# Optimization experiments

Hardware: AMD Instinct MI355X
Metric: run time of the kernel (lower is better)

The kernel has to match this reference:

```python
import jax, jax.numpy as jnp
import numpy as np

B, T, D, H = 128, 1024, 128, 128

def setup_inputs() -> dict:
    key = jax.random.key(0)
    ks = jax.random.split(key, 7)
    scale = 0.05
    return {
        "x": jax.random.normal(ks[0], (B, T, D), dtype=jnp.float32),
        "h0": jnp.zeros((B, H), dtype=jnp.float32),
        "U": jax.random.normal(ks[1], (D, H), dtype=jnp.float32) * scale,
        "W": jax.random.normal(ks[2], (H, H), dtype=jnp.float32) * scale,
        "V": jax.random.normal(ks[3], (H, H), dtype=jnp.float32) * scale,
        "bu": jnp.zeros((H,), dtype=jnp.float32),
        "bw": jnp.zeros((H,), dtype=jnp.float32),
        "bv": jnp.zeros((H,), dtype=jnp.float32),
    }

def reference(x, h0, U, W, V, bu, bw, bv):
    # Precompute input projection for all timesteps in one big GEMM: [B,T,H]
    xu = jnp.einsum('btd,dh->bth', x, U) + bu

    def step(h, xu_t):
        # st = tanh(x@U + bu + h@W + bw)
        st = jnp.tanh(xu_t + h @ W + bw)
        # o = tanh(st@V + bv)
        o = jnp.tanh(st @ V + bv)
        return st, o

    # scan over time: xu transposed to [T,B,H]
    _, o_seq = jax.lax.scan(step, h0, jnp.swapaxes(xu, 0, 1))
    return jnp.swapaxes(o_seq, 0, 1)  # [B,T,H]
```

## Files before the change

kernel.cpp:

```cpp
#include <hip/hip_runtime.h>

#define B_ 128
#define T_ 1024
#define D_ 128
#define H_ 128

typedef short bf16x8 __attribute__((ext_vector_type(8)));
typedef float f32x4 __attribute__((ext_vector_type(4)));

__device__ inline short f2bf(float f) {
    union { float f; unsigned u; } v; v.f = f;
    unsigned u = v.u;
    unsigned r = (u + 0x7fffu + ((u >> 16) & 1u)) >> 16;
    return (short)r;
}

__device__ inline float fast_tanh(float x) {
    float e = __expf(2.0f * x);
    return 1.0f - __fdividef(2.0f, 1.0f + e);
}

__device__ inline void lds_barrier() {
    asm volatile("s_waitcnt lgkmcnt(0)\n\ts_barrier" ::: "memory");
}

__global__ __launch_bounds__(256) void xu_kernel(
    const float* __restrict__ x, const float* __restrict__ U,
    const float* __restrict__ bu, float* __restrict__ out)
{
    __shared__ bf16x8 uf[2048];
    const int tid  = threadIdx.x;
    const int lane = tid & 63;
    const int wave = tid >> 6;
    const int q = lane >> 4, c = lane & 15;

    for (int s = tid; s < 2048; s += 256) {
        int l = s & 63, kk = (s >> 6) & 3, nt = s >> 8;
        int lq = l >> 4, lc = l & 15;
        int kbase = 32 * kk + 8 * lq;
        int col = 16 * nt + lc;
        bf16x8 f;
#pragma unroll
        for (int j = 0; j < 8; ++j)
            f[j] = f2bf(U[(kbase + j) * H_ + col]);
        uf[s] = f;
    }

    float bub[8];
#pragma unroll
    for (int nt = 0; nt < 8; ++nt) bub[nt] = bu[16 * nt + c];

    __syncthreads();

    for (int it = 0; it < 4; ++it) {
        const int row0 = (blockIdx.x * 4 + it) * 64 + wave * 16;

        bf16x8 af[4];
#pragma unroll
        for (int kk = 0; kk < 4; ++kk) {
            const float* px = x + (row0 + (lane & 15)) * D_ + 32 * kk + 8 * q;
            f32x4 a0 = *(const f32x4*)px;
            f32x4 a1 = *(const f32x4*)(px + 4);
            bf16x8 f;
            f[0] = f2bf(a0[0]); f[1] = f2bf(a0[1]); f[2] = f2bf(a0[2]); f[3] = f2bf(a0[3]);
            f[4] = f2bf(a1[0]); f[5] = f2bf(a1[1]); f[6] = f2bf(a1[2]); f[7] = f2bf(a1[3]);
            af[kk] = f;
        }

#pragma unroll
        for (int nt = 0; nt < 8; ++nt) {
            f32x4 acc = {bub[nt], bub[nt], bub[nt], bub[nt]};
#pragma unroll
            for (int kk = 0; kk < 4; ++kk)
                acc = __builtin_amdgcn_mfma_f32_16x16x32_bf16(af[kk], uf[(nt * 4 + kk) * 64 + lane], acc, 0, 0, 0);
            float* po = out + (row0 + 4 * q) * H_ + 16 * nt + c;
#pragma unroll
            for (int r = 0; r < 4; ++r)
                po[r * H_] = acc[r];
        }
    }
}

__global__ __launch_bounds__(1024) void scan_kernel(
    float* __restrict__ out,
    const float* __restrict__ h0,
    const float* __restrict__ W, const float* __restrict__ V,
    const float* __restrict__ bw, const float* __restrict__ bv)
{
    __shared__ __align__(16) short st[2][16][136];

    const int tid  = threadIdx.x;
    const int lane = tid & 63;
    const int wave = tid >> 6;
    const bool is_h = wave < 8;
    const int n  = wave & 7;
    const int q = lane >> 4, c = lane & 15;
    const int c0 = 16 * n;
    const int b0 = blockIdx.x * 16;

    const float* M = is_h ? W : V;
    bf16x8 wf[4];
#pragma unroll
    for (int kk = 0; kk < 4; ++kk) {
        int kbase = 32 * kk + 8 * q;
        bf16x8 f;
#pragma unroll
        for (int j = 0; j < 8; ++j)
            f[j] = f2bf(M[(kbase + j) * H_ + c0 + c]);
        wf[kk] = f;
    }
    const float vbias = is_h ? bw[c0 + c] : bv[c0 + c];

    {
        int m = wave;
        int k0 = lane * 2;
        const float* ph = h0 + (b0 + m) * H_ + k0;
        float2 hv = *(const float2*)ph;
        union { short s2[2]; unsigned u; } pk;
        pk.s2[0] = f2bf(hv.x);
        pk.s2[1] = f2bf(hv.y);
        *(unsigned*)&st[1][m][k0] = pk.u;
    }

    const int obase = (b0 + 4 * q) * T_ * H_ + c0 + c;

    f32x4 xubuf[8];
    if (is_h) {
#pragma unroll
        for (int u = 0; u < 8; ++u)
#pragma unroll
            for (int r = 0; r < 4; ++r)
                xubuf[u][r] = out[obase + r * T_ * H_ + u * H_];
    }
    lds_barrier();

    for (int tb = 0; tb < T_ / 8; ++tb) {
#pragma unroll
        for (int u = 0; u < 8; ++u) {
            const int t = tb * 8 + u;
            const int pr = (u + 1) & 1;
            const int pw = u & 1;

            if (is_h) {
                f32x4 xu_c = xubuf[u];
                if (t + 8 < T_) {
#pragma unroll
                    for (int r = 0; r < 4; ++r)
                        xubuf[u][r] = out[obase + r * T_ * H_ + (t + 8) * H_];
                }
                bf16x8 af[4];
#pragma unroll
                for (int kk = 0; kk < 4; ++kk)
                    af[kk] = *(const bf16x8*)&st[pr][lane & 15][32 * kk + 8 * q];
                f32x4 accA, accB;
#pragma unroll
                for (int r = 0; r < 4; ++r) { accA[r] = xu_c[r] + vbias; accB[r] = 0.f; }
                accA = __builtin_amdgcn_mfma_f32_16x16x32_bf16(af[0], wf[0], accA, 0, 0, 0);
                accB = __builtin_amdgcn_mfma_f32_16x16x32_bf16(af[1], wf[1], accB, 0, 0, 0);
                accA = __builtin_amdgcn_mfma_f32_16x16x32_bf16(af[2], wf[2], accA, 0, 0, 0);
                accB = __builtin_amdgcn_mfma_f32_16x16x32_bf16(af[3], wf[3], accB, 0, 0, 0);
#pragma unroll
                for (int r = 0; r < 4; ++r) {
                    float s = fast_tanh(accA[r] + accB[r]);
                    st[pw][4 * q + r][c0 + c] = f2bf(s);
                }
            } else if (t > 0) {
                bf16x8 af[4];
#pragma unroll
                for (int kk = 0; kk < 4; ++kk)
                    af[kk] = *(const bf16x8*)&st[pr][lane & 15][32 * kk + 8 * q];
                f32x4 acc = {vbias, vbias, vbias, vbias};
#pragma unroll
                for (int kk = 0; kk < 4; ++kk)
                    acc = __builtin_amdgcn_mfma_f32_16x16x32_bf16(af[kk], wf[kk], acc, 0, 0, 0);
#pragma unroll
                for (int r = 0; r < 4; ++r)
                    out[obase + r * T_ * H_ + (t - 1) * H_] = fast_tanh(acc[r]);
            }
            lds_barrier();
        }
    }

    if (!is_h) {
        bf16x8 af[4];
#pragma unroll
        for (int kk = 0; kk < 4; ++kk)
            af[kk] = *(const bf16x8*)&st[1][lane & 15][32 * kk + 8 * q];
        f32x4 acc = {vbias, vbias, vbias, vbias};
#pragma unroll
        for (int kk = 0; kk < 4; ++kk)
            acc = __builtin_amdgcn_mfma_f32_16x16x32_bf16(af[kk], wf[kk], acc, 0, 0, 0);
#pragma unroll
        for (int r = 0; r < 4; ++r)
            out[obase + r * T_ * H_ + (T_ - 1) * H_] = fast_tanh(acc[r]);
    }
}

extern "C" void kernel_launch(void* const* d_in, const int* in_sizes, int n_in,
                              void* d_out, int out_size, void* d_ws, size_t ws_size,
                              hipStream_t stream) {
    const float* x  = (const float*)d_in[0];
    const float* h0 = (const float*)d_in[1];
    const float* U  = (const float*)d_in[2];
    const float* W  = (const float*)d_in[3];
    const float* V  = (const float*)d_in[4];
    const float* bu = (const float*)d_in[5];
    const float* bw = (const float*)d_in[6];
    const float* bv = (const float*)d_in[7];
    float* out = (float*)d_out;

    xu_kernel<<<512, 256, 0, stream>>>(x, U, bu, out);
    scan_kernel<<<8, 1024, 0, stream>>>(out, h0, W, V, bw, bv);
}
```

Baseline: 896.5 us.

## Move output projection out of recurrent scan into separate parallel GEMM kernel

The serial scan kernel now computes only the hidden-state recurrence with 4 waves, each covering 32 columns. It writes bf16 hidden states in place into the output buffer, removing the V projection waves from the per-step critical path. A new o_kernel applies V, the bias and tanh as a fully parallel GEMM over all timesteps. Other changes fold bw into the xu precompute, use packed bf16 conversion instructions, switch tanh to exp2/rcp intrinsics and vectorize the output stores. The cost is an extra kernel launch and one more full pass over the output buffer.

Measured after the change: 850.3 us. 1.05x faster.

```diff
diff --git a/kernel.cpp b/kernel.cpp
--- a/kernel.cpp
+++ b/kernel.cpp
@@ -8,16 +8,16 @@
 typedef short bf16x8 __attribute__((ext_vector_type(8)));
 typedef float f32x4 __attribute__((ext_vector_type(4)));
 
-__device__ inline short f2bf(float f) {
-    union { float f; unsigned u; } v; v.f = f;
-    unsigned u = v.u;
-    unsigned r = (u + 0x7fffu + ((u >> 16) & 1u)) >> 16;
-    return (short)r;
+__device__ inline unsigned cvt_pk_bf16(float lo, float hi) {
+    unsigned r;
+    asm("v_cvt_pk_bf16_f32 %0, %1, %2" : "=v"(r) : "v"(lo), "v"(hi));
+    return r;
 }
 
 __device__ inline float fast_tanh(float x) {
-    float e = __expf(2.0f * x);
-    return 1.0f - __fdividef(2.0f, 1.0f + e);
+    float e = __builtin_amdgcn_exp2f(x * 2.885390081777927f);
+    float r = __builtin_amdgcn_rcpf(1.0f + e);
+    return fmaf(-2.0f, r, 1.0f);
 }
 
 __device__ inline void lds_barrier() {
@@ -26,7 +26,8 @@
 
 __global__ __launch_bounds__(256) void xu_kernel(
     const float* __restrict__ x, const float* __restrict__ U,
-    const float* __restrict__ bu, float* __restrict__ out)
+    const float* __restrict__ bu, const float* __restrict__ bw,
+    float* __restrict__ out)
 {
     __shared__ bf16x8 uf[2048];
     const int tid  = threadIdx.x;
@@ -39,99 +40,116 @@
         int lq = l >> 4, lc = l & 15;
         int kbase = 32 * kk + 8 * lq;
         int col = 16 * nt + lc;
-        bf16x8 f;
-#pragma unroll
-        for (int j = 0; j < 8; ++j)
-            f[j] = f2bf(U[(kbase + j) * H_ + col]);
-        uf[s] = f;
-    }
-
-    float bub[8];
-#pragma unroll
-    for (int nt = 0; nt < 8; ++nt) bub[nt] = bu[16 * nt + c];
+        float v[8];
+#pragma unroll
+        for (int j = 0; j < 8; ++j) v[j] = U[(kbase + j) * H_ + col];
+        union { bf16x8 v8; unsigned u[4]; } f;
+#pragma unroll
+        for (int j = 0; j < 4; ++j) f.u[j] = cvt_pk_bf16(v[2 * j], v[2 * j + 1]);
+        uf[s] = f.v8;
+    }
+
+    f32x4 bias4[8];
+#pragma unroll
+    for (int nt = 0; nt < 8; ++nt) {
+        const int cb = 16 * nt + 4 * q;
+        f32x4 a = *(const f32x4*)(bu + cb);
+        f32x4 b = *(const f32x4*)(bw + cb);
+#pragma unroll
+        for (int r = 0; r < 4; ++r) bias4[nt][r] = a[r] + b[r];
+    }
 
     __syncthreads();
 
     for (int it = 0; it < 4; ++it) {
         const int row0 = (blockIdx.x * 4 + it) * 64 + wave * 16;
-
         bf16x8 af[4];
 #pragma unroll
         for (int kk = 0; kk < 4; ++kk) {
-            const float* px = x + (row0 + (lane & 15)) * D_ + 32 * kk + 8 * q;
+            const float* px = x + (size_t)(row0 + c) * D_ + 32 * kk + 8 * q;
             f32x4 a0 = *(const f32x4*)px;
             f32x4 a1 = *(const f32x4*)(px + 4);
-            bf16x8 f;
-            f[0] = f2bf(a0[0]); f[1] = f2bf(a0[1]); f[2] = f2bf(a0[2]); f[3] = f2bf(a0[3]);
-            f[4] = f2bf(a1[0]); f[5] = f2bf(a1[1]); f[6] = f2bf(a1[2]); f[7] = f2bf(a1[3]);
-            af[kk] = f;
-        }
-
+            union { bf16x8 v8; unsigned u[4]; } f;
+            f.u[0] = cvt_pk_bf16(a0[0], a0[1]);
+            f.u[1] = cvt_pk_bf16(a0[2], a0[3]);
+            f.u[2] = cvt_pk_bf16(a1[0], a1[1]);
+            f.u[3] = cvt_pk_bf16(a1[2], a1[3]);
+            af[kk] = f.v8;
+        }
+        float* po = out + (size_t)(row0 + c) * H_ + 4 * q;
 #pragma unroll
         for (int nt = 0; nt < 8; ++nt) {
-            f32x4 acc = {bub[nt], bub[nt], bub[nt], bub[nt]};
+            f32x4 acc = bias4[nt];
 #pragma unroll
             for (int kk = 0; kk < 4; ++kk)
-                acc = __builtin_amdgcn_mfma_f32_16x16x32_bf16(af[kk], uf[(nt * 4 + kk) * 64 + lane], acc, 0, 0, 0);
-            float* po = out + (row0 + 4 * q) * H_ + 16 * nt + c;
-#pragma unroll
-            for (int r = 0; r < 4; ++r)
-                po[r * H_] = acc[r];
-        }
-    }
-}
-
-__global__ __launch_bounds__(1024) void scan_kernel(
-    float* __restrict__ out,
-    const float* __restrict__ h0,
-    const float* __restrict__ W, const float* __restrict__ V,
-    const float* __restrict__ bw, const float* __restrict__ bv)
+                acc = __builtin_amdgcn_mfma_f32_16x16x32_bf16(
+                    uf[(nt * 4 + kk) * 64 + lane], af[kk], acc, 0, 0, 0);
+            *(f32x4*)(po + 16 * nt) = acc;
+        }
+    }
+}
+
+__global__ __launch_bounds__(256) void scan_kernel(
+    float* __restrict__ out, const float* __restrict__ h0,
+    const float* __restrict__ W)
 {
     __shared__ __align__(16) short st[2][16][136];
 
     const int tid  = threadIdx.x;
     const int lane = tid & 63;
     const int wave = tid >> 6;
-    const bool is_h = wave < 8;
-    const int n  = wave & 7;
     const int q = lane >> 4, c = lane & 15;
-    const int c0 = 16 * n;
     const int b0 = blockIdx.x * 16;
-
-    const float* M = is_h ? W : V;
-    bf16x8 wf[4];
-#pragma unroll
-    for (int kk = 0; kk < 4; ++kk) {
-        int kbase = 32 * kk + 8 * q;
-        bf16x8 f;
-#pragma unroll
-        for (int j = 0; j < 8; ++j)
-            f[j] = f2bf(M[(kbase + j) * H_ + c0 + c]);
-        wf[kk] = f;
-    }
-    const float vbias = is_h ? bw[c0 + c] : bv[c0 + c];
+    const int cw = wave * 32 + 4 * q;
+
+    bf16x8 wf[2][4];
+#pragma unroll
+    for (int tt = 0; tt < 2; ++tt) {
+        const int c0 = wave * 32 + tt * 16;
+#pragma unroll
+        for (int kk = 0; kk < 4; ++kk) {
+            const int kbase = 32 * kk + 8 * q;
+            float v[8];
+#pragma unroll
+            for (int j = 0; j < 8; ++j) v[j] = W[(kbase + j) * H_ + c0 + c];
+            union { bf16x8 v8; unsigned u[4]; } f;
+#pragma unroll
+            for (int j = 0; j < 4; ++j) f.u[j] = cvt_pk_bf16(v[2 * j], v[2 * j + 1]);
+            wf[tt][kk] = f.v8;
+        }
+    }
 
     {
-        int m = wave;
-        int k0 = lane * 2;
-        const float* ph = h0 + (b0 + m) * H_ + k0;
-        float2 hv = *(const float2*)ph;
-        union { short s2[2]; unsigned u; } pk;
-        pk.s2[0] = f2bf(hv.x);
-        pk.s2[1] = f2bf(hv.y);
-        *(unsigned*)&st[1][m][k0] = pk.u;
-    }
-
-    const int obase = (b0 + 4 * q) * T_ * H_ + c0 + c;
-
-    f32x4 xubuf[8];
-    if (is_h) {
-#pragma unroll
-        for (int u = 0; u < 8; ++u)
-#pragma unroll
-            for (int r = 0; r < 4; ++r)
-                xubuf[u][r] = out[obase + r * T_ * H_ + u * H_];
-    }
+        const int m = tid >> 4, k0 = (tid & 15) * 8;
+        const float* ph = h0 + (size_t)(b0 + m) * H_ + k0;
+        f32x4 a0 = *(const f32x4*)ph;
+        f32x4 a1 = *(const f32x4*)(ph + 4);
+        union { bf16x8 v8; unsigned u[4]; } f;
+        f.u[0] = cvt_pk_bf16(a0[0], a0[1]);
+        f.u[1] = cvt_pk_bf16(a0[2], a0[3]);
+        f.u[2] = cvt_pk_bf16(a1[0], a1[1]);
+        f.u[3] = cvt_pk_bf16(a1[2], a1[3]);
+        *(bf16x8*)&st[1][m][k0] = f.v8;
+    }
+
+    const float* xup = out + ((size_t)(b0 + c) * T_) * H_ + cw;
+    f32x4 xub[8][2];
+    {
+        const float* pp = xup;
+#pragma unroll
+        for (int u = 0; u < 8; ++u) {
+            xub[u][0] = *(const f32x4*)pp;
+            xub[u][1] = *(const f32x4*)(pp + 16);
+            pp += H_;
+        }
+    }
+    const float* pf = xup + 8 * H_;
+
+    uint2 pkg0, pkg1;
+    char* pst = (char*)out + (((size_t)(b0 + c) * T_) * H_) * 4 + cw * 2;
+
+    const f32x4 z4 = {0.f, 0.f, 0.f, 0.f};
+
     lds_barrier();
 
     for (int tb = 0; tb < T_ / 8; ++tb) {
@@ -141,58 +159,108 @@
             const int pr = (u + 1) & 1;
             const int pw = u & 1;
 
-            if (is_h) {
-                f32x4 xu_c = xubuf[u];
-                if (t + 8 < T_) {
-#pragma unroll
-                    for (int r = 0; r < 4; ++r)
-                        xubuf[u][r] = out[obase + r * T_ * H_ + (t + 8) * H_];
-                }
-                bf16x8 af[4];
-#pragma unroll
-                for (int kk = 0; kk < 4; ++kk)
-                    af[kk] = *(const bf16x8*)&st[pr][lane & 15][32 * kk + 8 * q];
-                f32x4 accA, accB;
-#pragma unroll
-                for (int r = 0; r < 4; ++r) { accA[r] = xu_c[r] + vbias; accB[r] = 0.f; }
-                accA = __builtin_amdgcn_mfma_f32_16x16x32_bf16(af[0], wf[0], accA, 0, 0, 0);
-                accB = __builtin_amdgcn_mfma_f32_16x16x32_bf16(af[1], wf[1], accB, 0, 0, 0);
-                accA = __builtin_amdgcn_mfma_f32_16x16x32_bf16(af[2], wf[2], accA, 0, 0, 0);
-                accB = __builtin_amdgcn_mfma_f32_16x16x32_bf16(af[3], wf[3], accB, 0, 0, 0);
-#pragma unroll
-                for (int r = 0; r < 4; ++r) {
-                    float s = fast_tanh(accA[r] + accB[r]);
-                    st[pw][4 * q + r][c0 + c] = f2bf(s);
-                }
-            } else if (t > 0) {
-                bf16x8 af[4];
-#pragma unroll
-                for (int kk = 0; kk < 4; ++kk)
-                    af[kk] = *(const bf16x8*)&st[pr][lane & 15][32 * kk + 8 * q];
-                f32x4 acc = {vbias, vbias, vbias, vbias};
-#pragma unroll
-                for (int kk = 0; kk < 4; ++kk)
-                    acc = __builtin_amdgcn_mfma_f32_16x16x32_bf16(af[kk], wf[kk], acc, 0, 0, 0);
-#pragma unroll
-                for (int r = 0; r < 4; ++r)
-                    out[obase + r * T_ * H_ + (t - 1) * H_] = fast_tanh(acc[r]);
+            if (t > 0) {
+                *(uint2*)pst = pkg0;
+                *(uint2*)(pst + 32) = pkg1;
+                pst += H_ * 4;
             }
+
+            f32x4 xu0 = xub[u][0], xu1 = xub[u][1];
+            if (t < T_ - 8) {
+                xub[u][0] = *(const f32x4*)pf;
+                xub[u][1] = *(const f32x4*)(pf + 16);
+                pf += H_;
+            }
+
+            bf16x8 af[4];
+#pragma unroll
+            for (int kk = 0; kk < 4; ++kk)
+                af[kk] = *(const bf16x8*)&st[pr][c][32 * kk + 8 * q];
+
+            f32x4 aA = __builtin_amdgcn_mfma_f32_16x16x32_bf16(wf[0][0], af[0], xu0, 0, 0, 0);
+            f32x4 aB = __builtin_amdgcn_mfma_f32_16x16x32_bf16(wf[0][1], af[1], z4,  0, 0, 0);
+            f32x4 bA = __builtin_amdgcn_mfma_f32_16x16x32_bf16(wf[1][0], af[0], xu1, 0, 0, 0);
+            f32x4 bB = __builtin_amdgcn_mfma_f32_16x16x32_bf16(wf[1][1], af[1], z4,  0, 0, 0);
+            aA = __builtin_amdgcn_mfma_f32_16x16x32_bf16(wf[0][2], af[2], aA, 0, 0, 0);
+            aB = __builtin_amdgcn_mfma_f32_16x16x32_bf16(wf[0][3], af[3], aB, 0, 0, 0);
+            bA = __builtin_amdgcn_mfma_f32_16x16x32_bf16(wf[1][2], af[2], bA, 0, 0, 0);
+            bB = __builtin_amdgcn_mfma_f32_16x16x32_bf16(wf[1][3], af[3], bB, 0, 0, 0);
+
+            float s0 = fast_tanh(aA[0] + aB[0]);
+            float s1 = fast_tanh(aA[1] + aB[1]);
+            float s2 = fast_tanh(aA[2] + aB[2]);
+            float s3 = fast_tanh(aA[3] + aB[3]);
+            float s4 = fast_tanh(bA[0] + bB[0]);
+            float s5 = fast_tanh(bA[1] + bB[1]);
+            float s6 = fast_tanh(bA[2] + bB[2]);
+            float s7 = fast_tanh(bA[3] + bB[3]);
+
+            pkg0.x = cvt_pk_bf16(s0, s1);
+            pkg0.y = cvt_pk_bf16(s2, s3);
+            pkg1.x = cvt_pk_bf16(s4, s5);
+            pkg1.y = cvt_pk_bf16(s6, s7);
+
+            *(uint2*)&st[pw][c][cw]      = pkg0;
+            *(uint2*)&st[pw][c][cw + 16] = pkg1;
+
             lds_barrier();
         }
     }
-
-    if (!is_h) {
+    *(uint2*)pst = pkg0;
+    *(uint2*)(pst + 32) = pkg1;
+}
+
+__global__ __launch_bounds__(256) void o_kernel(
+    float* __restrict__ out, const float* __restrict__ V,
+    const float* __restrict__ bv)
+{
+    __shared__ bf16x8 vf[2048];
+    const int tid  = threadIdx.x;
+    const int lane = tid & 63;
+    const int wave = tid >> 6;
+    const int q = lane >> 4, c = lane & 15;
+
+    for (int s = tid; s < 2048; s += 256) {
+        int l = s & 63, kk = (s >> 6) & 3, nt = s >> 8;
+        int lq = l >> 4, lc = l & 15;
+        int kbase = 32 * kk + 8 * lq;
+        int col = 16 * nt + lc;
+        float v[8];
+#pragma unroll
+        for (int j = 0; j < 8; ++j) v[j] = V[(kbase + j) * H_ + col];
+        union { bf16x8 v8; unsigned u[4]; } f;
+#pragma unroll
+        for (int j = 0; j < 4; ++j) f.u[j] = cvt_pk_bf16(v[2 * j], v[2 * j + 1]);
+        vf[s] = f.v8;
+    }
+
+    f32x4 bias4[8];
+#pragma unroll
+    for (int nt = 0; nt < 8; ++nt)
+        bias4[nt] = *(const f32x4*)(bv + 16 * nt + 4 * q);
+
+    __syncthreads();
+
+    for (int it = 0; it < 4; ++it) {
+        const int row0 = (blockIdx.x * 4 + it) * 64 + wave * 16;
+        const char* pa = (const char*)out + (size_t)(row0 + c) * (H_ * 4);
         bf16x8 af[4];
 #pragma unroll
         for (int kk = 0; kk < 4; ++kk)
-            af[kk] = *(const bf16x8*)&st[1][lane & 15][32 * kk + 8 * q];
-        f32x4 acc = {vbias, vbias, vbias, vbias};
-#pragma unroll
-        for (int kk = 0; kk < 4; ++kk)
-            acc = __builtin_amdgcn_mfma_f32_16x16x32_bf16(af[kk], wf[kk], acc, 0, 0, 0);
-#pragma unroll
-        for (int r = 0; r < 4; ++r)
-            out[obase + r * T_ * H_ + (T_ - 1) * H_] = fast_tanh(acc[r]);
+            af[kk] = *(const bf16x8*)(pa + 64 * kk + 16 * q);
+        float* po = out + (size_t)(row0 + c) * H_ + 4 * q;
+#pragma unroll
+        for (int nt = 0; nt < 8; ++nt) {
+            f32x4 acc = bias4[nt];
+#pragma unroll
+            for (int kk = 0; kk < 4; ++kk)
+                acc = __builtin_amdgcn_mfma_f32_16x16x32_bf16(
+                    vf[(nt * 4 + kk) * 64 + lane], af[kk], acc, 0, 0, 0);
+            f32x4 o;
+#pragma unroll
+            for (int r = 0; r < 4; ++r) o[r] = fast_tanh(acc[r]);
+            *(f32x4*)(po + 16 * nt) = o;
+        }
     }
 }
 
@@ -209,6 +277,7 @@
     const float* bv = (const float*)d_in[7];
     float* out = (float*)d_out;
 
-    xu_kernel<<<512, 256, 0, stream>>>(x, U, bu, out);
-    scan_kernel<<<8, 1024, 0, stream>>>(out, h0, W, V, bw, bv);
-}
+    xu_kernel<<<512, 256, 0, stream>>>(x, U, bu, bw, out);
+    scan_kernel<<<8, 256, 0, stream>>>(out, h0, W);
+    o_kernel<<<512, 256, 0, stream>>>(out, V, bv);
+}
```
